# Kernel optimization log

Measured on AMD Instinct MI355X. Metric: run time of the kernel, lower is better.

The kernel has to match this reference:

```python
import jax, jax.numpy as jnp
import numpy as np

NUM_TOKENS = 16384
COMPACT = 8192
HIDDEN = 2048
INTER = 8192


def setup_inputs() -> dict:
    key = jax.random.key(0)
    k_x, k_fg, k_sc, k_wg, k_wu, k_wd = jax.random.split(key, 6)
    x = jax.random.normal(k_x, (NUM_TOKENS, HIDDEN), dtype=jnp.float32)
    fold_gather = jax.random.randint(k_fg, (COMPACT,), 0, NUM_TOKENS, dtype=jnp.int32)
    scatter_indices = jax.random.randint(k_sc, (NUM_TOKENS,), 0, COMPACT, dtype=jnp.int32)
    # torch nn.Linear weights are [out_features, in_features]
    s_h = 1.0 / np.sqrt(HIDDEN)
    s_i = 1.0 / np.sqrt(INTER)
    W_gate = jax.random.uniform(k_wg, (INTER, HIDDEN), jnp.float32, -s_h, s_h)
    W_up = jax.random.uniform(k_wu, (INTER, HIDDEN), jnp.float32, -s_h, s_h)
    W_down = jax.random.uniform(k_wd, (HIDDEN, INTER), jnp.float32, -s_i, s_i)
    return {"x": x, "W_gate": W_gate, "W_up": W_up, "W_down": W_down,
            "fold_gather": fold_gather, "scatter_indices": scatter_indices}


def reference(x, W_gate, W_up, W_down, fold_gather, scatter_indices):
    # gather original tokens into compact space
    x_compact = jnp.take(x, fold_gather, axis=0)               # [C, H]
    gate = jax.nn.silu(jnp.einsum('ch,ih->ci', x_compact, W_gate))  # [C, I]
    up = jnp.einsum('ch,ih->ci', x_compact, W_up)               # [C, I]
    down = jnp.einsum('ci,hi->ch', gate * up, W_down)           # [C, H]
    # scatter compact results back to every original token slot
    return jnp.take(down, scatter_indices, axis=0)              # [N, H]
```

## Files before the change

kernel.cpp:

```cpp
#include <hip/hip_runtime.h>
#include <hip/hip_bf16.h>
#include <stdint.h>

#define HIDDEN  2048
#define INTER   8192
#define COMPACT 8192
#define NTOK    16384

typedef unsigned short ushort_t;
typedef float  f32x4  __attribute__((ext_vector_type(4)));
typedef __bf16 bf16x8 __attribute__((ext_vector_type(8)));

__device__ __align__(16) ushort_t g_xc[(size_t)COMPACT * HIDDEN];
__device__ __align__(16) ushort_t g_wg[(size_t)INTER * HIDDEN];
__device__ __align__(16) ushort_t g_wu[(size_t)INTER * HIDDEN];
__device__ __align__(16) ushort_t g_wd[(size_t)HIDDEN * INTER];
__device__ __align__(16) float    g_dn[(size_t)COMPACT * HIDDEN];

__device__ __forceinline__ ushort_t f2bf(float f) {
    uint32_t u = __builtin_bit_cast(uint32_t, f);
    uint32_t lsb = (u >> 16) & 1u;
    u += 0x7fffu + lsb;
    return (ushort_t)(u >> 16);
}

__device__ __forceinline__ void async_cp16(const void* g, void* l) {
    __builtin_amdgcn_global_load_lds(
        (__attribute__((address_space(1))) void*)((void*)g),
        (__attribute__((address_space(3))) void*)l,
        16, 0, 0);
}

__global__ __launch_bounds__(256)
void k_gather_cast(const float* __restrict__ x, const int* __restrict__ fg)
{
    const int c = blockIdx.x;
    const int t = threadIdx.x;
    const float4* src = (const float4*)(x + (size_t)fg[c] * HIDDEN) + (t << 1);
    float4 a = src[0], b = src[1];
    union { ushort_t u[8]; uint4 v; } p;
    p.u[0] = f2bf(a.x); p.u[1] = f2bf(a.y); p.u[2] = f2bf(a.z); p.u[3] = f2bf(a.w);
    p.u[4] = f2bf(b.x); p.u[5] = f2bf(b.y); p.u[6] = f2bf(b.z); p.u[7] = f2bf(b.w);
    *((uint4*)(g_xc + (size_t)c * HIDDEN) + t) = p.v;
}

template<int W>
__global__ __launch_bounds__(256)
void k_cast(const float* __restrict__ src)
{
    ushort_t* __restrict__ dst = (W == 0) ? g_wg : (W == 1) ? g_wu : g_wd;
    const size_t g = (size_t)blockIdx.x * 256 + threadIdx.x;
    const float4* s = (const float4*)src + (g << 1);
    float4 a = s[0], b = s[1];
    union { ushort_t u[8]; uint4 v; } p;
    p.u[0] = f2bf(a.x); p.u[1] = f2bf(a.y); p.u[2] = f2bf(a.z); p.u[3] = f2bf(a.w);
    p.u[4] = f2bf(b.x); p.u[5] = f2bf(b.y); p.u[6] = f2bf(b.z); p.u[7] = f2bf(b.w);
    *((uint4*)dst + g) = p.v;
}

__global__ __launch_bounds__(256, 2)
void k_gateup(ushort_t* __restrict__ h)
{
    __shared__ __align__(16) ushort_t As[128 * 32];
    __shared__ __align__(16) ushort_t Bg[128 * 32];
    __shared__ __align__(16) ushort_t Bu[128 * 32];

    const int tid = threadIdx.x;
    const int bm0 = blockIdx.y << 7;
    const int bn0 = blockIdx.x << 7;

    const int sr = tid >> 2;
    const int sc = (tid & 3) << 3;

    const ushort_t* pa0 = g_xc + (size_t)(bm0 + sr) * HIDDEN + sc;
    const ushort_t* pa1 = pa0 + (size_t)64 * HIDDEN;
    const ushort_t* pg0 = g_wg + (size_t)(bn0 + sr) * HIDDEN + sc;
    const ushort_t* pg1 = pg0 + (size_t)64 * HIDDEN;
    const ushort_t* pu0 = g_wu + (size_t)(bn0 + sr) * HIDDEN + sc;
    const ushort_t* pu1 = pu0 + (size_t)64 * HIDDEN;

    ushort_t* lA0 = &As[tid << 3];
    ushort_t* lA1 = &As[(tid + 256) << 3];
    ushort_t* lG0 = &Bg[tid << 3];
    ushort_t* lG1 = &Bg[(tid + 256) << 3];
    ushort_t* lU0 = &Bu[tid << 3];
    ushort_t* lU1 = &Bu[(tid + 256) << 3];

    const int lane = tid & 63;
    const int wv = tid >> 6;
    const int wm = (wv & 1) << 6;
    const int wn = (wv >> 1) << 6;
    const int lr = lane & 15;
    const int kq = (lane >> 4) << 3;

    f32x4 accg[4][4], accu[4][4];
    #pragma unroll
    for (int i = 0; i < 4; ++i)
        #pragma unroll
        for (int j = 0; j < 4; ++j) {
            accg[i][j] = (f32x4){0.f, 0.f, 0.f, 0.f};
            accu[i][j] = (f32x4){0.f, 0.f, 0.f, 0.f};
        }

    for (int k0 = 0; k0 < HIDDEN; k0 += 32) {
        async_cp16(pa0, lA0); async_cp16(pa1, lA1);
        async_cp16(pg0, lG0); async_cp16(pg1, lG1);
        async_cp16(pu0, lU0); async_cp16(pu1, lU1);
        pa0 += 32; pa1 += 32; pg0 += 32; pg1 += 32; pu0 += 32; pu1 += 32;
        __syncthreads();

        bf16x8 af[4], gf[4], uf[4];
        #pragma unroll
        for (int i = 0; i < 4; ++i) {
            af[i] = *(const bf16x8*)&As[(wm + (i << 4) + lr) * 32 + kq];
            gf[i] = *(const bf16x8*)&Bg[(wn + (i << 4) + lr) * 32 + kq];
            uf[i] = *(const bf16x8*)&Bu[(wn + (i << 4) + lr) * 32 + kq];
        }
        #pragma unroll
        for (int i = 0; i < 4; ++i)
            #pragma unroll
            for (int j = 0; j < 4; ++j) {
                accg[i][j] = __builtin_amdgcn_mfma_f32_16x16x32_bf16(af[i], gf[j], accg[i][j], 0, 0, 0);
                accu[i][j] = __builtin_amdgcn_mfma_f32_16x16x32_bf16(af[i], uf[j], accu[i][j], 0, 0, 0);
            }
        __syncthreads();
    }

    const int orow0 = bm0 + wm + ((lane >> 4) << 2);
    const int ocol  = bn0 + wn + lr;
    #pragma unroll
    for (int i = 0; i < 4; ++i)
        #pragma unroll
        for (int j = 0; j < 4; ++j)
            #pragma unroll
            for (int r = 0; r < 4; ++r) {
                float g = accg[i][j][r];
                float u = accu[i][j][r];
                float s = g / (1.0f + __expf(-g));
                size_t off = (size_t)(orow0 + (i << 4) + r) * INTER + (size_t)(ocol + (j << 4));
                h[off] = f2bf(s * u);
            }
}

__global__ __launch_bounds__(256, 2)
void k_down(const ushort_t* __restrict__ hbuf)
{
    __shared__ __align__(16) ushort_t As[128 * 32];
    __shared__ __align__(16) ushort_t Bs[128 * 32];

    const int tid = threadIdx.x;
    const int bm0 = blockIdx.y << 7;
    const int bn0 = blockIdx.x << 7;
    const int sr = tid >> 2;
    const int sc = (tid & 3) << 3;

    const ushort_t* pa0 = hbuf + (size_t)(bm0 + sr) * INTER + sc;
    const ushort_t* pa1 = pa0 + (size_t)64 * INTER;
    const ushort_t* pb0 = g_wd + (size_t)(bn0 + sr) * INTER + sc;
    const ushort_t* pb1 = pb0 + (size_t)64 * INTER;

    ushort_t* lA0 = &As[tid << 3];
    ushort_t* lA1 = &As[(tid + 256) << 3];
    ushort_t* lB0 = &Bs[tid << 3];
    ushort_t* lB1 = &Bs[(tid + 256) << 3];

    const int lane = tid & 63;
    const int wv = tid >> 6;
    const int wm = (wv & 1) << 6;
    const int wn = (wv >> 1) << 6;
    const int lr = lane & 15;
    const int kq = (lane >> 4) << 3;

    f32x4 acc[4][4];
    #pragma unroll
    for (int i = 0; i < 4; ++i)
        #pragma unroll
        for (int j = 0; j < 4; ++j)
            acc[i][j] = (f32x4){0.f, 0.f, 0.f, 0.f};

    for (int k0 = 0; k0 < INTER; k0 += 32) {
        async_cp16(pa0, lA0); async_cp16(pa1, lA1);
        async_cp16(pb0, lB0); async_cp16(pb1, lB1);
        pa0 += 32; pa1 += 32; pb0 += 32; pb1 += 32;
        __syncthreads();

        bf16x8 af[4], bfr[4];
        #pragma unroll
        for (int i = 0; i < 4; ++i) {
            af[i]  = *(const bf16x8*)&As[(wm + (i << 4) + lr) * 32 + kq];
            bfr[i] = *(const bf16x8*)&Bs[(wn + (i << 4) + lr) * 32 + kq];
        }
        #pragma unroll
        for (int i = 0; i < 4; ++i)
            #pragma unroll
            for (int j = 0; j < 4; ++j)
                acc[i][j] = __builtin_amdgcn_mfma_f32_16x16x32_bf16(af[i], bfr[j], acc[i][j], 0, 0, 0);
        __syncthreads();
    }

    const int orow0 = bm0 + wm + ((lane >> 4) << 2);
    const int ocol  = bn0 + wn + lr;
    #pragma unroll
    for (int i = 0; i < 4; ++i)
        #pragma unroll
        for (int j = 0; j < 4; ++j)
            #pragma unroll
            for (int r = 0; r < 4; ++r) {
                size_t off = (size_t)(orow0 + (i << 4) + r) * HIDDEN + (size_t)(ocol + (j << 4));
                g_dn[off] = acc[i][j][r];
            }
}

__global__ __launch_bounds__(256)
void k_scatter(const int* __restrict__ sc,
               float4* __restrict__ out)
{
    const int gid = blockIdx.x * 256 + threadIdx.x;
    const int row = gid >> 9;
    const int ch  = gid & 511;
    const int s = sc[row];
    out[((size_t)row << 9) + ch] = ((const float4*)g_dn)[((size_t)s << 9) + ch];
}

extern "C" void kernel_launch(void* const* d_in, const int* in_sizes, int n_in,
                              void* d_out, int out_size, void* d_ws, size_t ws_size,
                              hipStream_t stream)
{
    (void)in_sizes; (void)n_in; (void)out_size; (void)d_ws; (void)ws_size;

    const float* x  = (const float*)d_in[0];
    const float* Wg = (const float*)d_in[1];
    const float* Wu = (const float*)d_in[2];
    const float* Wd = (const float*)d_in[3];
    const int* fg = (const int*)d_in[4];
    const int* sc = (const int*)d_in[5];
    float* out = (float*)d_out;

    ushort_t* h = (ushort_t*)d_out;

    k_gather_cast<<<COMPACT, 256, 0, stream>>>(x, fg);
    k_cast<0><<<(INTER * HIDDEN / 8) / 256, 256, 0, stream>>>(Wg);
    k_cast<1><<<(INTER * HIDDEN / 8) / 256, 256, 0, stream>>>(Wu);
    k_cast<2><<<(HIDDEN * INTER / 8) / 256, 256, 0, stream>>>(Wd);

    k_gateup<<<dim3(INTER / 128, COMPACT / 128), 256, 0, stream>>>(h);
    k_down<<<dim3(HIDDEN / 128, COMPACT / 128), 256, 0, stream>>>(h);
    k_scatter<<<(NTOK * HIDDEN / 4) / 256, 256, 0, stream>>>(
        sc, (float4*)out);
}
```

Before: 1.498 ms.

## Rewrite GEMM kernels with 256-row tiles, double-buffered LDS pipeline and swizzle

Both GEMM kernels move to 512-thread blocks with larger tiles (256x128 for gate/up, 256x256 for down) and a K step of 64. Global-to-LDS loads are double-buffered and interleaved with four MFMA phases, using explicit vmcnt waits, raw barriers and setprio. LDS uses an XOR-swizzled layout to avoid bank conflicts. The aim is to hide memory latency and raise MFMA utilisation. The cost is a much larger LDS footprint, higher register pressure and fragile hand-counted wait logic.

```diff
diff --git a/kernel.cpp b/kernel.cpp
--- a/kernel.cpp
+++ b/kernel.cpp
@@ -7,9 +7,16 @@
 #define COMPACT 8192
 #define NTOK    16384
 
+#define NT_GU (HIDDEN / 64)
+#define NT_DN (INTER / 64)
+
 typedef unsigned short ushort_t;
 typedef float  f32x4  __attribute__((ext_vector_type(4)));
 typedef __bf16 bf16x8 __attribute__((ext_vector_type(8)));
+
+#define VMCNT(n) asm volatile("s_waitcnt vmcnt(" #n ")" ::: "memory")
+#define FENCE()  asm volatile("" ::: "memory")
+#define BARRIER() do { FENCE(); __builtin_amdgcn_s_barrier(); FENCE(); } while (0)
 
 __device__ __align__(16) ushort_t g_xc[(size_t)COMPACT * HIDDEN];
 __device__ __align__(16) ushort_t g_wg[(size_t)INTER * HIDDEN];
@@ -29,6 +36,10 @@
         (__attribute__((address_space(1))) void*)((void*)g),
         (__attribute__((address_space(3))) void*)l,
         16, 0, 0);
+}
+
+__device__ __forceinline__ bf16x8 ldfrag(const ushort_t* m, int row, int slot) {
+    return *(const bf16x8*)(m + row * 64 + slot * 8);
 }
 
 __global__ __launch_bounds__(256)
@@ -58,157 +69,323 @@
     *((uint4*)dst + g) = p.v;
 }
 
-__global__ __launch_bounds__(256, 2)
+#define MFMA16(ACC, AF, BF)                                                    \
+    _Pragma("unroll")                                                          \
+    for (int i = 0; i < 4; ++i)                                                \
+        _Pragma("unroll")                                                      \
+        for (int j = 0; j < 2; ++j) {                                          \
+            ACC[i][j] = __builtin_amdgcn_mfma_f32_16x16x32_bf16(AF[i][0], BF[j][0], ACC[i][j], 0, 0, 0); \
+            ACC[i][j] = __builtin_amdgcn_mfma_f32_16x16x32_bf16(AF[i][1], BF[j][1], ACC[i][j], 0, 0, 0); \
+        }
+
+__global__ __launch_bounds__(512, 2)
 void k_gateup(ushort_t* __restrict__ h)
 {
-    __shared__ __align__(16) ushort_t As[128 * 32];
-    __shared__ __align__(16) ushort_t Bg[128 * 32];
-    __shared__ __align__(16) ushort_t Bu[128 * 32];
-
-    const int tid = threadIdx.x;
-    const int bm0 = blockIdx.y << 7;
+    __shared__ __align__(16) ushort_t As[2][256 * 64];
+    __shared__ __align__(16) ushort_t Gs[2][128 * 64];
+    __shared__ __align__(16) ushort_t Us[2][128 * 64];
+
+    const int tid  = threadIdx.x;
+    const int lane = tid & 63;
+    const int wv   = tid >> 6;
+    const int wr   = wv >> 2;
+    const int wc   = wv & 3;
+    const int lr   = lane & 15;
+    const int q    = lane >> 4;
+    const int sl0  = q ^ (lr & 7);
+    const int sl1  = sl0 ^ 4;
+    const int srow = tid >> 3;
+    const int scol = ((lane & 7) ^ (lane >> 3)) << 3;
+    const int lofs = tid * 8;
+
+    const int bm0 = blockIdx.y << 8;
     const int bn0 = blockIdx.x << 7;
 
-    const int sr = tid >> 2;
-    const int sc = (tid & 3) << 3;
-
-    const ushort_t* pa0 = g_xc + (size_t)(bm0 + sr) * HIDDEN + sc;
-    const ushort_t* pa1 = pa0 + (size_t)64 * HIDDEN;
-    const ushort_t* pg0 = g_wg + (size_t)(bn0 + sr) * HIDDEN + sc;
-    const ushort_t* pg1 = pg0 + (size_t)64 * HIDDEN;
-    const ushort_t* pu0 = g_wu + (size_t)(bn0 + sr) * HIDDEN + sc;
-    const ushort_t* pu1 = pu0 + (size_t)64 * HIDDEN;
-
-    ushort_t* lA0 = &As[tid << 3];
-    ushort_t* lA1 = &As[(tid + 256) << 3];
-    ushort_t* lG0 = &Bg[tid << 3];
-    ushort_t* lG1 = &Bg[(tid + 256) << 3];
-    ushort_t* lU0 = &Bu[tid << 3];
-    ushort_t* lU1 = &Bu[(tid + 256) << 3];
-
-    const int lane = tid & 63;
-    const int wv = tid >> 6;
-    const int wm = (wv & 1) << 6;
-    const int wn = (wv >> 1) << 6;
-    const int lr = lane & 15;
-    const int kq = (lane >> 4) << 3;
-
-    f32x4 accg[4][4], accu[4][4];
+    const ushort_t* pA = g_xc + (size_t)(bm0 + srow) * HIDDEN + scol;
+    const ushort_t* pG = g_wg + (size_t)(bn0 + srow) * HIDDEN + scol;
+    const ushort_t* pU = g_wu + (size_t)(bn0 + srow) * HIDDEN + scol;
+    const size_t rS = (size_t)64 * HIDDEN;
+
+    f32x4 ag0[4][2], ag1[4][2], au0[4][2], au1[4][2];
     #pragma unroll
     for (int i = 0; i < 4; ++i)
         #pragma unroll
-        for (int j = 0; j < 4; ++j) {
-            accg[i][j] = (f32x4){0.f, 0.f, 0.f, 0.f};
-            accu[i][j] = (f32x4){0.f, 0.f, 0.f, 0.f};
-        }
-
-    for (int k0 = 0; k0 < HIDDEN; k0 += 32) {
-        async_cp16(pa0, lA0); async_cp16(pa1, lA1);
-        async_cp16(pg0, lG0); async_cp16(pg1, lG1);
-        async_cp16(pu0, lU0); async_cp16(pu1, lU1);
-        pa0 += 32; pa1 += 32; pg0 += 32; pg1 += 32; pu0 += 32; pu1 += 32;
-        __syncthreads();
-
-        bf16x8 af[4], gf[4], uf[4];
+        for (int j = 0; j < 2; ++j) {
+            ag0[i][j] = (f32x4){0.f,0.f,0.f,0.f};
+            ag1[i][j] = (f32x4){0.f,0.f,0.f,0.f};
+            au0[i][j] = (f32x4){0.f,0.f,0.f,0.f};
+            au1[i][j] = (f32x4){0.f,0.f,0.f,0.f};
+        }
+
+    {
+        ushort_t* An = As[0]; ushort_t* Gn = Gs[0]; ushort_t* Un = Us[0];
+        async_cp16(pA,          An + lofs);
+        async_cp16(pA + rS,     An + 4096 + lofs);
+        async_cp16(pG,          Gn + lofs);
+        async_cp16(pG + rS,     Gn + 4096 + lofs);
+        async_cp16(pU,          Un + lofs);
+        async_cp16(pU + rS,     Un + 4096 + lofs);
+        async_cp16(pA + 2*rS,   An + 8192 + lofs);
+        async_cp16(pA + 3*rS,   An + 12288 + lofs);
+        pA += 64; pG += 64; pU += 64;
+        VMCNT(0);
+        BARRIER();
+    }
+
+    for (int t = 0; t < NT_GU; ++t) {
+        const ushort_t* Ac = As[t & 1];
+        const ushort_t* Gc = Gs[t & 1];
+        const ushort_t* Uc = Us[t & 1];
+        ushort_t* An = As[(t & 1) ^ 1];
+        ushort_t* Gn = Gs[(t & 1) ^ 1];
+        ushort_t* Un = Us[(t & 1) ^ 1];
+        const bool more = (t + 1 < NT_GU);
+
+        bf16x8 af[4][2], bg[2][2], bu[2][2];
+
         #pragma unroll
         for (int i = 0; i < 4; ++i) {
-            af[i] = *(const bf16x8*)&As[(wm + (i << 4) + lr) * 32 + kq];
-            gf[i] = *(const bf16x8*)&Bg[(wn + (i << 4) + lr) * 32 + kq];
-            uf[i] = *(const bf16x8*)&Bu[(wn + (i << 4) + lr) * 32 + kq];
-        }
-        #pragma unroll
-        for (int i = 0; i < 4; ++i)
-            #pragma unroll
-            for (int j = 0; j < 4; ++j) {
-                accg[i][j] = __builtin_amdgcn_mfma_f32_16x16x32_bf16(af[i], gf[j], accg[i][j], 0, 0, 0);
-                accu[i][j] = __builtin_amdgcn_mfma_f32_16x16x32_bf16(af[i], uf[j], accu[i][j], 0, 0, 0);
-            }
-        __syncthreads();
+            const int row = wr * 64 + i * 16 + lr;
+            af[i][0] = ldfrag(Ac, row, sl0);
+            af[i][1] = ldfrag(Ac, row, sl1);
+        }
+        #pragma unroll
+        for (int j = 0; j < 2; ++j) {
+            const int row = wc * 32 + j * 16 + lr;
+            bg[j][0] = ldfrag(Gc, row, sl0);
+            bg[j][1] = ldfrag(Gc, row, sl1);
+        }
+        if (more) {
+            async_cp16(pA,      An + lofs);
+            async_cp16(pA + rS, An + 4096 + lofs);
+            VMCNT(4);
+        } else {
+            VMCNT(2);
+        }
+        BARRIER();
+        __builtin_amdgcn_s_setprio(1);
+        MFMA16(ag0, af, bg);
+        __builtin_amdgcn_s_setprio(0);
+        BARRIER();
+
+        #pragma unroll
+        for (int j = 0; j < 2; ++j) {
+            const int row = wc * 32 + j * 16 + lr;
+            bu[j][0] = ldfrag(Uc, row, sl0);
+            bu[j][1] = ldfrag(Uc, row, sl1);
+        }
+        if (more) {
+            async_cp16(pG,      Gn + lofs);
+            async_cp16(pG + rS, Gn + 4096 + lofs);
+            VMCNT(4);
+        } else {
+            VMCNT(0);
+        }
+        BARRIER();
+        __builtin_amdgcn_s_setprio(1);
+        MFMA16(au0, af, bu);
+        __builtin_amdgcn_s_setprio(0);
+        BARRIER();
+
+        #pragma unroll
+        for (int i = 0; i < 4; ++i) {
+            const int row = 128 + wr * 64 + i * 16 + lr;
+            af[i][0] = ldfrag(Ac, row, sl0);
+            af[i][1] = ldfrag(Ac, row, sl1);
+        }
+        if (more) {
+            async_cp16(pU,      Un + lofs);
+            async_cp16(pU + rS, Un + 4096 + lofs);
+        }
+        BARRIER();
+        __builtin_amdgcn_s_setprio(1);
+        MFMA16(ag1, af, bg);
+        __builtin_amdgcn_s_setprio(0);
+        BARRIER();
+
+        if (more) {
+            async_cp16(pA + 2*rS, An + 8192 + lofs);
+            async_cp16(pA + 3*rS, An + 12288 + lofs);
+        }
+        VMCNT(4);
+        BARRIER();
+        __builtin_amdgcn_s_setprio(1);
+        MFMA16(au1, af, bu);
+        __builtin_amdgcn_s_setprio(0);
+        BARRIER();
+
+        pA += 64; pG += 64; pU += 64;
     }
 
-    const int orow0 = bm0 + wm + ((lane >> 4) << 2);
-    const int ocol  = bn0 + wn + lr;
+    const int or0 = bm0 + wr * 64 + (q << 2);
+    const int oc  = bn0 + wc * 32 + lr;
+    #define GU_STORE(AG, AU, MH)                                               \
+        _Pragma("unroll")                                                      \
+        for (int i = 0; i < 4; ++i)                                            \
+            _Pragma("unroll")                                                  \
+            for (int j = 0; j < 2; ++j)                                        \
+                _Pragma("unroll")                                              \
+                for (int r = 0; r < 4; ++r) {                                  \
+                    float g = AG[i][j][r];                                     \
+                    float u = AU[i][j][r];                                     \
+                    float s = g / (1.0f + __expf(-g));                         \
+                    h[(size_t)(or0 + (MH)*128 + i*16 + r) * INTER + (oc + j*16)] = f2bf(s * u); \
+                }
+    GU_STORE(ag0, au0, 0)
+    GU_STORE(ag1, au1, 1)
+    #undef GU_STORE
+}
+
+__global__ __launch_bounds__(512, 2)
+void k_down(const ushort_t* __restrict__ hbuf)
+{
+    __shared__ __align__(16) ushort_t As[2][256 * 64];
+    __shared__ __align__(16) ushort_t Bs[2][256 * 64];
+
+    const int tid  = threadIdx.x;
+    const int lane = tid & 63;
+    const int wv   = tid >> 6;
+    const int wr   = wv >> 2;
+    const int wc   = wv & 3;
+    const int lr   = lane & 15;
+    const int q    = lane >> 4;
+    const int sl0  = q ^ (lr & 7);
+    const int sl1  = sl0 ^ 4;
+    const int srow = tid >> 3;
+    const int scol = ((lane & 7) ^ (lane >> 3)) << 3;
+    const int lofs = tid * 8;
+
+    const int bm0 = blockIdx.y << 8;
+    const int bn0 = blockIdx.x << 8;
+
+    const ushort_t* pH = hbuf + (size_t)(bm0 + srow) * INTER + scol;
+    const ushort_t* pW = g_wd + (size_t)(bn0 + srow) * INTER + scol;
+    const size_t rS = (size_t)64 * INTER;
+
+    f32x4 c00[4][2], c01[4][2], c10[4][2], c11[4][2];
     #pragma unroll
     for (int i = 0; i < 4; ++i)
         #pragma unroll
-        for (int j = 0; j < 4; ++j)
-            #pragma unroll
-            for (int r = 0; r < 4; ++r) {
-                float g = accg[i][j][r];
-                float u = accu[i][j][r];
-                float s = g / (1.0f + __expf(-g));
-                size_t off = (size_t)(orow0 + (i << 4) + r) * INTER + (size_t)(ocol + (j << 4));
-                h[off] = f2bf(s * u);
-            }
-}
-
-__global__ __launch_bounds__(256, 2)
-void k_down(const ushort_t* __restrict__ hbuf)
-{
-    __shared__ __align__(16) ushort_t As[128 * 32];
-    __shared__ __align__(16) ushort_t Bs[128 * 32];
-
-    const int tid = threadIdx.x;
-    const int bm0 = blockIdx.y << 7;
-    const int bn0 = blockIdx.x << 7;
-    const int sr = tid >> 2;
-    const int sc = (tid & 3) << 3;
-
-    const ushort_t* pa0 = hbuf + (size_t)(bm0 + sr) * INTER + sc;
-    const ushort_t* pa1 = pa0 + (size_t)64 * INTER;
-    const ushort_t* pb0 = g_wd + (size_t)(bn0 + sr) * INTER + sc;
-    const ushort_t* pb1 = pb0 + (size_t)64 * INTER;
-
-    ushort_t* lA0 = &As[tid << 3];
-    ushort_t* lA1 = &As[(tid + 256) << 3];
-    ushort_t* lB0 = &Bs[tid << 3];
-    ushort_t* lB1 = &Bs[(tid + 256) << 3];
-
-    const int lane = tid & 63;
-    const int wv = tid >> 6;
-    const int wm = (wv & 1) << 6;
-    const int wn = (wv >> 1) << 6;
-    const int lr = lane & 15;
-    const int kq = (lane >> 4) << 3;
-
-    f32x4 acc[4][4];
-    #pragma unroll
-    for (int i = 0; i < 4; ++i)
-        #pragma unroll
-        for (int j = 0; j < 4; ++j)
-            acc[i][j] = (f32x4){0.f, 0.f, 0.f, 0.f};
-
-    for (int k0 = 0; k0 < INTER; k0 += 32) {
-        async_cp16(pa0, lA0); async_cp16(pa1, lA1);
-        async_cp16(pb0, lB0); async_cp16(pb1, lB1);
-        pa0 += 32; pa1 += 32; pb0 += 32; pb1 += 32;
-        __syncthreads();
-
-        bf16x8 af[4], bfr[4];
+        for (int j = 0; j < 2; ++j) {
+            c00[i][j] = (f32x4){0.f,0.f,0.f,0.f};
+            c01[i][j] = (f32x4){0.f,0.f,0.f,0.f};
+            c10[i][j] = (f32x4){0.f,0.f,0.f,0.f};
+            c11[i][j] = (f32x4){0.f,0.f,0.f,0.f};
+        }
+
+    {
+        ushort_t* An = As[0]; ushort_t* Bn = Bs[0];
+        async_cp16(pH,          An + lofs);
+        async_cp16(pH + rS,     An + 4096 + lofs);
+        async_cp16(pW,          Bn + lofs);
+        async_cp16(pW + rS,     Bn + 4096 + lofs);
+        async_cp16(pW + 2*rS,   Bn + 8192 + lofs);
+        async_cp16(pW + 3*rS,   Bn + 12288 + lofs);
+        async_cp16(pH + 2*rS,   An + 8192 + lofs);
+        async_cp16(pH + 3*rS,   An + 12288 + lofs);
+        pH += 64; pW += 64;
+        VMCNT(0);
+        BARRIER();
+    }
+
+    for (int t = 0; t < NT_DN; ++t) {
+        const ushort_t* Ac = As[t & 1];
+        const ushort_t* Bc = Bs[t & 1];
+        ushort_t* An = As[(t & 1) ^ 1];
+        ushort_t* Bn = Bs[(t & 1) ^ 1];
+        const bool more = (t + 1 < NT_DN);
+
+        bf16x8 af[4][2], b0[2][2], b1[2][2];
+
         #pragma unroll
         for (int i = 0; i < 4; ++i) {
-            af[i]  = *(const bf16x8*)&As[(wm + (i << 4) + lr) * 32 + kq];
-            bfr[i] = *(const bf16x8*)&Bs[(wn + (i << 4) + lr) * 32 + kq];
-        }
-        #pragma unroll
-        for (int i = 0; i < 4; ++i)
-            #pragma unroll
-            for (int j = 0; j < 4; ++j)
-                acc[i][j] = __builtin_amdgcn_mfma_f32_16x16x32_bf16(af[i], bfr[j], acc[i][j], 0, 0, 0);
-        __syncthreads();
+            const int row = wr * 64 + i * 16 + lr;
+            af[i][0] = ldfrag(Ac, row, sl0);
+            af[i][1] = ldfrag(Ac, row, sl1);
+        }
+        #pragma unroll
+        for (int j = 0; j < 2; ++j) {
+            const int row = wc * 32 + j * 16 + lr;
+            b0[j][0] = ldfrag(Bc, row, sl0);
+            b0[j][1] = ldfrag(Bc, row, sl1);
+        }
+        if (more) {
+            async_cp16(pH,      An + lofs);
+            async_cp16(pH + rS, An + 4096 + lofs);
+            VMCNT(4);
+        } else {
+            VMCNT(2);
+        }
+        BARRIER();
+        __builtin_amdgcn_s_setprio(1);
+        MFMA16(c00, af, b0);
+        __builtin_amdgcn_s_setprio(0);
+        BARRIER();
+
+        #pragma unroll
+        for (int j = 0; j < 2; ++j) {
+            const int row = 128 + wc * 32 + j * 16 + lr;
+            b1[j][0] = ldfrag(Bc, row, sl0);
+            b1[j][1] = ldfrag(Bc, row, sl1);
+        }
+        if (more) {
+            async_cp16(pW,      Bn + lofs);
+            async_cp16(pW + rS, Bn + 4096 + lofs);
+            VMCNT(4);
+        } else {
+            VMCNT(0);
+        }
+        BARRIER();
+        __builtin_amdgcn_s_setprio(1);
+        MFMA16(c01, af, b1);
+        __builtin_amdgcn_s_setprio(0);
+        BARRIER();
+
+        #pragma unroll
+        for (int i = 0; i < 4; ++i) {
+            const int row = 128 + wr * 64 + i * 16 + lr;
+            af[i][0] = ldfrag(Ac, row, sl0);
+            af[i][1] = ldfrag(Ac, row, sl1);
+        }
+        if (more) {
+            async_cp16(pW + 2*rS, Bn + 8192 + lofs);
+            async_cp16(pW + 3*rS, Bn + 12288 + lofs);
+        }
+        BARRIER();
+        __builtin_amdgcn_s_setprio(1);
+        MFMA16(c10, af, b0);
+        __builtin_amdgcn_s_setprio(0);
+        BARRIER();
+
+        if (more) {
+            async_cp16(pH + 2*rS, An + 8192 + lofs);
+            async_cp16(pH + 3*rS, An + 12288 + lofs);
+        }
+        VMCNT(4);
+        BARRIER();
+        __builtin_amdgcn_s_setprio(1);
+        MFMA16(c11, af, b1);
+        __builtin_amdgcn_s_setprio(0);
+        BARRIER();
+
+        pH += 64; pW += 64;
     }
 
-    const int orow0 = bm0 + wm + ((lane >> 4) << 2);
-    const int ocol  = bn0 + wn + lr;
-    #pragma unroll
-    for (int i = 0; i < 4; ++i)
-        #pragma unroll
-        for (int j = 0; j < 4; ++j)
-            #pragma unroll
-            for (int r = 0; r < 4; ++r) {
-                size_t off = (size_t)(orow0 + (i << 4) + r) * HIDDEN + (size_t)(ocol + (j << 4));
-                g_dn[off] = acc[i][j][r];
-            }
+    const int or0 = bm0 + wr * 64 + (q << 2);
+    const int oc  = bn0 + wc * 32 + lr;
+    #define DN_STORE(CC, MH, NH)                                               \
+        _Pragma("unroll")                                                      \
+        for (int i = 0; i < 4; ++i)                                            \
+            _Pragma("unroll")                                                  \
+            for (int j = 0; j < 2; ++j)                                        \
+                _Pragma("unroll")                                              \
+                for (int r = 0; r < 4; ++r)                                    \
+                    g_dn[(size_t)(or0 + (MH)*128 + i*16 + r) * HIDDEN + (oc + (NH)*128 + j*16)] = CC[i][j][r];
+    DN_STORE(c00, 0, 0)
+    DN_STORE(c01, 0, 1)
+    DN_STORE(c10, 1, 0)
+    DN_STORE(c11, 1, 1)
+    #undef DN_STORE
 }
 
 __global__ __launch_bounds__(256)
@@ -243,8 +420,8 @@
     k_cast<1><<<(INTER * HIDDEN / 8) / 256, 256, 0, stream>>>(Wu);
     k_cast<2><<<(HIDDEN * INTER / 8) / 256, 256, 0, stream>>>(Wd);
 
-    k_gateup<<<dim3(INTER / 128, COMPACT / 128), 256, 0, stream>>>(h);
-    k_down<<<dim3(HIDDEN / 128, COMPACT / 128), 256, 0, stream>>>(h);
+    k_gateup<<<dim3(INTER / 128, COMPACT / 256), 512, 0, stream>>>(h);
+    k_down<<<dim3(HIDDEN / 256, COMPACT / 256), 512, 0, stream>>>(h);
     k_scatter<<<(NTOK * HIDDEN / 4) / 256, 256, 0, stream>>>(
         sc, (float4*)out);
 }
```

Measured after the change: 1.377 ms. 8.1% less time.
